# Performance work log

Measured on AMD Instinct MI355X. Metric: run time of the kernel, lower is better.

Reference implementation:

```python
import jax, jax.numpy as jnp
import numpy as np

B, T, C = 4, 2048, 1024
H = 16
D = C // H  # head_dim = 64


def setup_inputs() -> dict:
    key = jax.random.key(0)
    k1, k2, k3 = jax.random.split(key, 3)
    x = jax.random.normal(k1, (B, T, C), dtype=jnp.float32)
    w_qkv = jax.random.normal(k2, (C, 3 * C), dtype=jnp.float32) * (1.0 / np.sqrt(C))
    b_qkv = jnp.zeros((3 * C,), dtype=jnp.float32)
    w_out = jax.random.normal(k3, (C, C), dtype=jnp.float32) * (1.0 / np.sqrt(C))
    b_out = jnp.zeros((C,), dtype=jnp.float32)
    return {"x": x, "w_qkv": w_qkv, "b_qkv": b_qkv, "w_out": w_out, "b_out": b_out}


def reference(x, w_qkv, b_qkv, w_out, b_out):
    # QKV projection: [B,T,3C]
    qkv = x @ w_qkv + b_qkv
    q, k, v = jnp.split(qkv, 3, axis=-1)
    # [B,H,T,D]
    q = q.reshape(B, T, H, D).transpose(0, 2, 1, 3)
    k = k.reshape(B, T, H, D).transpose(0, 2, 1, 3)
    v = v.reshape(B, T, H, D).transpose(0, 2, 1, 3)
    scale = 1.0 / np.sqrt(D)
    # scores: [B,H,T,T]
    scores = jnp.einsum("bhqd,bhkd->bhqk", q, k) * scale
    causal = jnp.tril(jnp.ones((T, T), dtype=bool))
    scores = jnp.where(causal[None, None, :, :], scores, -jnp.inf)
    attn = jax.nn.softmax(scores, axis=-1)
    out = jnp.einsum("bhqk,bhkd->bhqd", attn, v)
    out = out.transpose(0, 2, 1, 3).reshape(B, T, C)
    return out @ w_out + b_out
```

## Files before the change

kernel.cpp:

```cpp
#include <hip/hip_runtime.h>
#include <hip/hip_bf16.h>

#define BB 4
#define TT 2048
#define CC 1024
#define HH 16
#define DD 64

typedef __attribute__((ext_vector_type(8))) short short8;
typedef __attribute__((ext_vector_type(4))) float f32x4;

__device__ __forceinline__ float bf2f(short s) {
  unsigned u = ((unsigned)(unsigned short)s) << 16;
  float f;
  __builtin_memcpy(&f, &u, 4);
  return f;
}
__device__ __forceinline__ short f2bf(float f) {
  unsigned u;
  __builtin_memcpy(&u, &f, 4);
  u = (u + 0x7fffu + ((u >> 16) & 1u)) >> 16;
  return (short)u;
}

__device__ __forceinline__ unsigned cvt_pk_bf16(float lo, float hi) {
  unsigned r;
  asm("v_cvt_pk_bf16_f32 %0, %1, %2" : "=v"(r) : "v"(lo), "v"(hi));
  return r;
}

__device__ __forceinline__ float exp2_fast(float x) {
  float r;
  asm("v_exp_f32 %0, %1" : "=v"(r) : "v"(x));
  return r;
}

template <int CTRL>
__device__ __forceinline__ float dpp_f(float v) {
  union { float f; int i; } u;
  u.f = v;
  u.i = __builtin_amdgcn_update_dpp(0, u.i, CTRL, 0xf, 0xf, true);
  return u.f;
}
__device__ __forceinline__ float rowmax16(float v) {
  v = fmaxf(v, dpp_f<0x128>(v));
  v = fmaxf(v, dpp_f<0x124>(v));
  v = fmaxf(v, dpp_f<0x4E>(v));
  v = fmaxf(v, dpp_f<0xB1>(v));
  return v;
}
__device__ __forceinline__ float rowsum16(float v) {
  v += dpp_f<0x128>(v);
  v += dpp_f<0x124>(v);
  v += dpp_f<0x4E>(v);
  v += dpp_f<0xB1>(v);
  return v;
}

__device__ __forceinline__ void gload_lds16(const void* g, void* l) {
  __builtin_amdgcn_global_load_lds(
      (const __attribute__((address_space(1))) void*)g,
      (__attribute__((address_space(3))) void*)l, 16, 0, 0);
}

__global__ __launch_bounds__(256) void cast_bf16_kernel(
    const float* __restrict__ in, short* __restrict__ out, int n) {
  int i = (blockIdx.x * 256 + threadIdx.x) * 4;
  if (i >= n) return;
  float4 v = *(const float4*)&in[i];
  short4 o;
  o.x = f2bf(v.x); o.y = f2bf(v.y); o.z = f2bf(v.z); o.w = f2bf(v.w);
  *(short4*)&out[i] = o;
}

__global__ __launch_bounds__(256) void transpose_cast_kernel(
    const float* __restrict__ in, short* __restrict__ out, int R, int Cc) {
  __shared__ float tile[32][33];
  const int tx = threadIdx.x, ty = threadIdx.y;
  const int c0 = blockIdx.x * 32, r0 = blockIdx.y * 32;
#pragma unroll
  for (int i = 0; i < 32; i += 8)
    tile[ty + i][tx] = in[(size_t)(r0 + ty + i) * Cc + c0 + tx];
  __syncthreads();
#pragma unroll
  for (int i = 0; i < 32; i += 8)
    out[(size_t)(c0 + ty + i) * R + r0 + tx] = f2bf(tile[tx][ty + i]);
}

__global__ __launch_bounds__(256) void v_transpose_kernel(
    const short* __restrict__ vb, short* __restrict__ vt) {
  __shared__ int tile[32][33];
  const int tx = threadIdx.x, ty = threadIdx.y;
  const int bh = blockIdx.z;
  const int d0 = blockIdx.x * 32, t0 = blockIdx.y * 32;
  const short* src = vb + (size_t)bh * TT * DD;
  short* dstp = vt + (size_t)bh * DD * TT;
#pragma unroll
  for (int i = 0; i < 32; i += 8)
    tile[ty + i][tx] = src[(size_t)(t0 + ty + i) * DD + d0 + tx];
  __syncthreads();
#pragma unroll
  for (int i = 0; i < 32; i += 8)
    dstp[(size_t)(d0 + ty + i) * TT + t0 + tx] = (short)tile[tx][ty + i];
}

template <int MODE>
__global__ __launch_bounds__(256) void gemm_bf16(
    const short* __restrict__ A, const short* __restrict__ Bt,
    const float* __restrict__ bias, float* __restrict__ outF,
    short* __restrict__ outQ, short* __restrict__ outK, short* __restrict__ outV,
    int M, int N, int K) {
  __shared__ __align__(16) short As[2][128 * 32];
  __shared__ __align__(16) short Bs[2][128 * 32];
  const int tid = threadIdx.x;
  const int lane = tid & 63, wid = tid >> 6;
  const int wm = wid >> 1, wn = wid & 1;
  const int nbx = N >> 7;
  const int nwg = nbx * (M >> 7);
  const int lin0 = blockIdx.x;
  const int lin = (lin0 & 7) * (nwg >> 3) + (lin0 >> 3);
  const int bx = lin % nbx, by = lin / nbx;
  const int row0 = by * 128, col0 = bx * 128;
  const int fr = lane & 15, fq = lane >> 4;
  const short* Ab = A + (size_t)row0 * K;
  const short* Bb = Bt + (size_t)col0 * K;
  const int sr = tid >> 2;
  const int so = (tid & 3) * 8;

  f32x4 acc[4][4];
#pragma unroll
  for (int m = 0; m < 4; ++m)
#pragma unroll
    for (int n = 0; n < 4; ++n) {
      f32x4 z = {0.f, 0.f, 0.f, 0.f};
      acc[m][n] = z;
    }

#define GSTAGE(c, k0)                                                          \
  do {                                                                         \
    gload_lds16(Ab + (size_t)sr * K + (k0) + so, &As[c][tid * 8]);             \
    gload_lds16(Ab + (size_t)(sr + 64) * K + (k0) + so, &As[c][2048 + tid * 8]); \
    gload_lds16(Bb + (size_t)sr * K + (k0) + so, &Bs[c][tid * 8]);             \
    gload_lds16(Bb + (size_t)(sr + 64) * K + (k0) + so, &Bs[c][2048 + tid * 8]); \
  } while (0)

  GSTAGE(0, 0);
  const int nkt = K >> 5;
  for (int kt = 0; kt < nkt; ++kt) {
    const int cur = kt & 1;
    asm volatile("s_waitcnt vmcnt(0)" ::: "memory");
    __builtin_amdgcn_s_barrier();
    if (kt + 1 < nkt) GSTAGE(cur ^ 1, (kt + 1) * 32);
    short8 a[4], b[4];
#pragma unroll
    for (int m = 0; m < 4; ++m)
      a[m] = *(const short8*)&As[cur][(wm * 64 + m * 16 + fr) * 32 + fq * 8];
#pragma unroll
    for (int n = 0; n < 4; ++n)
      b[n] = *(const short8*)&Bs[cur][(wn * 64 + n * 16 + fr) * 32 + fq * 8];
    __builtin_amdgcn_s_setprio(1);
#pragma unroll
    for (int m = 0; m < 4; ++m)
#pragma unroll
      for (int n = 0; n < 4; ++n)
        acc[m][n] = __builtin_amdgcn_mfma_f32_16x16x32_bf16(a[m], b[n], acc[m][n], 0, 0, 0);
    __builtin_amdgcn_s_setprio(0);
  }

  float bv[4];
#pragma unroll
  for (int n = 0; n < 4; ++n) bv[n] = bias[col0 + wn * 64 + n * 16 + fr];

  if (MODE == 0) {
#pragma unroll
    for (int m = 0; m < 4; ++m) {
      const int grow = row0 + wm * 64 + m * 16 + fq * 4;
#pragma unroll
      for (int n = 0; n < 4; ++n) {
        const int gcol = col0 + wn * 64 + n * 16 + fr;
#pragma unroll
        for (int r = 0; r < 4; ++r)
          outF[(size_t)(grow + r) * N + gcol] = acc[m][n][r] + bv[n];
      }
    }
  } else {
#pragma unroll
    for (int n = 0; n < 4; ++n) {
      const int gcol = col0 + wn * 64 + n * 16 + fr;
      const int which = gcol >> 10;
      const int h = (gcol & 1023) >> 6;
      const int d = gcol & 63;
      short* dst = (which == 0) ? outQ : (which == 1) ? outK : outV;
#pragma unroll
      for (int m = 0; m < 4; ++m) {
        const int grow = row0 + wm * 64 + m * 16 + fq * 4;
#pragma unroll
        for (int r = 0; r < 4; ++r) {
          const int gb = (grow + r) >> 11;
          const int gt = (grow + r) & 2047;
          const int bh = gb * HH + h;
          dst[((size_t)bh * TT + gt) * DD + d] = f2bf(acc[m][n][r] + bv[n]);
        }
      }
    }
  }
}

#define C2 0.18033688f

__global__ __launch_bounds__(256) void attn_mfma_kernel(
    const short* __restrict__ q,
    const short* __restrict__ k,
    const short* __restrict__ vt,
    short* __restrict__ ctx) {
  __shared__ __align__(16) short Ks[2][128 * 64];
  __shared__ __align__(16) short Vs[2][64 * 128];
  __shared__ __align__(16) short Ps[4][32 * 64];
  const int tid = threadIdx.x, lane = tid & 63, wid = tid >> 6;
  const int fr = lane & 15, fq = lane >> 4;
  const int lin = blockIdx.x;
  const int bh = lin & 63;
  const int qt = 15 - (lin >> 6);
  const int q0 = qt * 128;
  const int qw0 = q0 + wid * 32;
  const short* kbp = k + (size_t)bh * TT * DD;
  const short* vbp = vt + (size_t)bh * DD * TT;
  char* PsB = (char*)&Ps[wid][0];

#define KSB(c) ((char*)&Ks[0][0] + (c) * (128 * 64 * 2))
#define VSB(c) ((char*)&Vs[0][0] + (c) * (64 * 128 * 2))

  short8 aq[2][2];
#pragma unroll
  for (int m = 0; m < 2; ++m)
#pragma unroll
    for (int ks = 0; ks < 2; ++ks)
      aq[m][ks] = *(const short8*)&q[((size_t)bh * TT + qw0 + m * 16 + fr) * DD + ks * 32 + fq * 8];

  float M[2][4], L[2][4];
  f32x4 o[2][4];
#pragma unroll
  for (int m = 0; m < 2; ++m)
#pragma unroll
    for (int r = 0; r < 4; ++r) { M[m][r] = -1e30f; L[m][r] = 0.f; }
#pragma unroll
  for (int m = 0; m < 2; ++m)
#pragma unroll
    for (int dg = 0; dg < 4; ++dg) {
      f32x4 z = {0.f, 0.f, 0.f, 0.f};
      o[m][dg] = z;
    }

  const int nt = qt + 1;

#define STAGE(c, tt)                                                           \
  do {                                                                         \
    const int kv0_ = (tt) * 128;                                               \
    _Pragma("unroll") for (int b_ = 0; b_ < 4; ++b_) {                         \
      const int lo_ = b_ * 4096 + tid * 16;                                    \
      const int row_ = lo_ >> 7;                                               \
      const int colb_ = lo_ & 127;                                             \
      const int src_ = colb_ ^ ((row_ & 7) << 4);                              \
      gload_lds16(kbp + ((size_t)(kv0_ + row_)) * DD + (src_ >> 1),            \
                  KSB(c) + lo_);                                               \
    }                                                                          \
    _Pragma("unroll") for (int b_ = 0; b_ < 4; ++b_) {                         \
      const int lo_ = b_ * 4096 + tid * 16;                                    \
      const int row_ = lo_ >> 8;                                               \
      const int colb_ = lo_ & 255;                                             \
      const int src_ = colb_ ^ ((row_ & 7) << 4);                              \
      gload_lds16(vbp + (size_t)row_ * TT + kv0_ + (src_ >> 1),                \
                  VSB(c) + lo_);                                               \
    }                                                                          \
  } while (0)

  STAGE(0, 0);

  for (int t = 0; t < nt; ++t) {
    const int cur = t & 1;
    asm volatile("s_waitcnt vmcnt(0)" ::: "memory");
    __builtin_amdgcn_s_barrier();
    if (t + 1 < nt) STAGE(cur ^ 1, t + 1);
    const int kv0 = t * 128;
    if (kv0 > qw0 + 31) continue;

#pragma unroll
    for (int sub = 0; sub < 2; ++sub) {
      const int kv0s = kv0 + sub * 64;
      if (kv0s > qw0 + 31) continue;
      const bool domask = (kv0s + 63 > qw0);

      short8 bk[4][2];
#pragma unroll
      for (int n = 0; n < 4; ++n) {
        const int row = sub * 64 + n * 16 + fr;
#pragma unroll
        for (int ks = 0; ks < 2; ++ks)
          bk[n][ks] = *(const short8*)(KSB(cur) + row * 128 +
                                       (((ks * 64 + fq * 16) ^ ((row & 7) << 4))));
      }
      f32x4 s[2][4];
      __builtin_amdgcn_s_setprio(1);
#pragma unroll
      for (int m = 0; m < 2; ++m)
#pragma unroll
        for (int n = 0; n < 4; ++n) {
          f32x4 z = {0.f, 0.f, 0.f, 0.f};
          s[m][n] = z;
#pragma unroll
          for (int ks = 0; ks < 2; ++ks)
            s[m][n] = __builtin_amdgcn_mfma_f32_16x16x32_bf16(aq[m][ks], bk[n][ks], s[m][n], 0, 0, 0);
        }
      __builtin_amdgcn_s_setprio(0);

      if (domask) {
#pragma unroll
        for (int m = 0; m < 2; ++m)
#pragma unroll
          for (int n = 0; n < 4; ++n)
#pragma unroll
            for (int r = 0; r < 4; ++r) {
              const int qq = qw0 + m * 16 + fq * 4 + r;
              const int kk = kv0s + n * 16 + fr;
              if (kk > qq) s[m][n][r] = -1e30f;
            }
      }

#pragma unroll
      for (int m = 0; m < 2; ++m) {
        float rm2[4];
#pragma unroll
        for (int r = 0; r < 4; ++r) {
          float rm = fmaxf(fmaxf(s[m][0][r], s[m][1][r]), fmaxf(s[m][2][r], s[m][3][r]));
          rm2[r] = rowmax16(rm) * C2;
        }
        float dmax = fmaxf(fmaxf(rm2[0] - M[m][0], rm2[1] - M[m][1]),
                           fmaxf(rm2[2] - M[m][2], rm2[3] - M[m][3]));
        if (__any(dmax > 8.0f)) {
#pragma unroll
          for (int r = 0; r < 4; ++r) {
            const float Mn = fmaxf(M[m][r], rm2[r]);
            const float corr = exp2_fast(M[m][r] - Mn);
            M[m][r] = Mn;
            L[m][r] *= corr;
#pragma unroll
            for (int dg = 0; dg < 4; ++dg) o[m][dg][r] *= corr;
          }
        }
        float psum[4] = {0.f, 0.f, 0.f, 0.f};
        const int brow = m * 16 + fq * 4;
        unsigned short* pw = (unsigned short*)PsB;
#pragma unroll
        for (int n = 0; n < 4; ++n) {
          const float p0 = exp2_fast(__builtin_fmaf(s[m][n][0], C2, -M[m][0]));
          const float p1 = exp2_fast(__builtin_fmaf(s[m][n][1], C2, -M[m][1]));
          const float p2 = exp2_fast(__builtin_fmaf(s[m][n][2], C2, -M[m][2]));
          const float p3 = exp2_fast(__builtin_fmaf(s[m][n][3], C2, -M[m][3]));
          psum[0] += p0; psum[1] += p1; psum[2] += p2; psum[3] += p3;
          const unsigned u0 = cvt_pk_bf16(p0, p1);
          const unsigned u1 = cvt_pk_bf16(p2, p3);
          const int colb = n * 32 + fr * 2;
          pw[((brow + 0) * 128 + (colb ^ (((brow + 0) & 7) << 4))) >> 1] = (unsigned short)u0;
          pw[((brow + 1) * 128 + (colb ^ (((brow + 1) & 7) << 4))) >> 1] = (unsigned short)(u0 >> 16);
          pw[((brow + 2) * 128 + (colb ^ (((brow + 2) & 7) << 4))) >> 1] = (unsigned short)u1;
          pw[((brow + 3) * 128 + (colb ^ (((brow + 3) & 7) << 4))) >> 1] = (unsigned short)(u1 >> 16);
        }
#pragma unroll
        for (int r = 0; r < 4; ++r) L[m][r] += rowsum16(psum[r]);
      }

      short8 ap[2][2], bv[4][2];
#pragma unroll
      for (int m = 0; m < 2; ++m) {
        const int qrow = m * 16 + fr;
#pragma unroll
        for (int ks = 0; ks < 2; ++ks)
          ap[m][ks] = *(const short8*)(PsB + qrow * 128 +
                                       (((ks * 64 + fq * 16) ^ ((qrow & 7) << 4))));
      }
#pragma unroll
      for (int dg = 0; dg < 4; ++dg) {
        const int row = dg * 16 + fr;
#pragma unroll
        for (int ks = 0; ks < 2; ++ks)
          bv[dg][ks] = *(const short8*)(VSB(cur) + row * 256 +
                                        (((sub * 128 + ks * 64 + fq * 16) ^ ((row & 7) << 4))));
      }
      __builtin_amdgcn_s_setprio(1);
#pragma unroll
      for (int m = 0; m < 2; ++m)
#pragma unroll
        for (int dg = 0; dg < 4; ++dg)
#pragma unroll
          for (int ks = 0; ks < 2; ++ks)
            o[m][dg] = __builtin_amdgcn_mfma_f32_16x16x32_bf16(ap[m][ks], bv[dg][ks], o[m][dg], 0, 0, 0);
      __builtin_amdgcn_s_setprio(0);
    }
  }

  const int b = bh >> 4, h = bh & 15;
#pragma unroll
  for (int m = 0; m < 2; ++m)
#pragma unroll
    for (int dg = 0; dg < 4; ++dg)
#pragma unroll
      for (int r = 0; r < 4; ++r) {
        const int qq = qw0 + m * 16 + fq * 4 + r;
        ctx[((size_t)(b * TT + qq)) * CC + h * DD + dg * 16 + fr] =
            f2bf(o[m][dg][r] / L[m][r]);
      }
}

extern "C" void kernel_launch(void* const* d_in, const int* in_sizes, int n_in,
                              void* d_out, int out_size, void* d_ws, size_t ws_size,
                              hipStream_t stream) {
  (void)in_sizes; (void)n_in; (void)out_size; (void)ws_size;
  const float* x = (const float*)d_in[0];
  const float* w_qkv = (const float*)d_in[1];
  const float* b_qkv = (const float*)d_in[2];
  const float* w_out = (const float*)d_in[3];
  const float* b_out = (const float*)d_in[4];
  float* out = (float*)d_out;

  char* w = (char*)d_ws;
  short* xb    = (short*)w; w += (size_t)BB * TT * CC * 2;
  short* wqkvT = (short*)w; w += (size_t)3 * CC * CC * 2;
  short* woutT = (short*)w; w += (size_t)CC * CC * 2;
  short* qb    = (short*)w; w += (size_t)BB * HH * TT * DD * 2;
  short* kb    = (short*)w; w += (size_t)BB * HH * TT * DD * 2;
  short* vtb   = (short*)w; w += (size_t)BB * HH * DD * TT * 2;
  short* ctx   = (short*)w; w += (size_t)BB * TT * CC * 2;

  const int M = BB * TT;

  cast_bf16_kernel<<<dim3((M * CC) / 4 / 256), dim3(256), 0, stream>>>(x, xb, M * CC);
  transpose_cast_kernel<<<dim3(3 * CC / 32, CC / 32), dim3(32, 8), 0, stream>>>(
      w_qkv, wqkvT, CC, 3 * CC);
  transpose_cast_kernel<<<dim3(CC / 32, CC / 32), dim3(32, 8), 0, stream>>>(
      w_out, woutT, CC, CC);

  gemm_bf16<1><<<dim3((3 * CC / 128) * (M / 128)), dim3(256), 0, stream>>>(
      xb, wqkvT, b_qkv, nullptr, qb, kb, ctx, M, 3 * CC, CC);

  v_transpose_kernel<<<dim3(DD / 32, TT / 32, BB * HH), dim3(32, 8), 0, stream>>>(
      ctx, vtb);

  attn_mfma_kernel<<<dim3(16 * 64), dim3(256), 0, stream>>>(qb, kb, vtb, ctx);

  gemm_bf16<0><<<dim3((CC / 128) * (M / 128)), dim3(256), 0, stream>>>(
      ctx, woutT, b_out, out, nullptr, nullptr, nullptr, M, CC, CC);
}
```

Measured before the change: 287.8 us.

## Swizzle GEMM LDS tiles and shrink attention KV tiles to 64

```diff
diff --git a/kernel.cpp b/kernel.cpp
--- a/kernel.cpp
+++ b/kernel.cpp
@@ -125,7 +125,8 @@
   const short* Ab = A + (size_t)row0 * K;
   const short* Bb = Bt + (size_t)col0 * K;
   const int sr = tid >> 2;
-  const int so = (tid & 3) * 8;
+  const int ssl = (((tid & 3) ^ (sr & 3)) * 8);
+  const int rsl = ((fq ^ (fr & 3)) * 8);
 
   f32x4 acc[4][4];
 #pragma unroll
@@ -136,12 +137,12 @@
       acc[m][n] = z;
     }
 
-#define GSTAGE(c, k0)                                                          \
-  do {                                                                         \
-    gload_lds16(Ab + (size_t)sr * K + (k0) + so, &As[c][tid * 8]);             \
-    gload_lds16(Ab + (size_t)(sr + 64) * K + (k0) + so, &As[c][2048 + tid * 8]); \
-    gload_lds16(Bb + (size_t)sr * K + (k0) + so, &Bs[c][tid * 8]);             \
-    gload_lds16(Bb + (size_t)(sr + 64) * K + (k0) + so, &Bs[c][2048 + tid * 8]); \
+#define GSTAGE(c, k0)                                                            \
+  do {                                                                           \
+    gload_lds16(Ab + (size_t)sr * K + (k0) + ssl, &As[c][tid * 8]);              \
+    gload_lds16(Ab + (size_t)(sr + 64) * K + (k0) + ssl, &As[c][2048 + tid * 8]);\
+    gload_lds16(Bb + (size_t)sr * K + (k0) + ssl, &Bs[c][tid * 8]);              \
+    gload_lds16(Bb + (size_t)(sr + 64) * K + (k0) + ssl, &Bs[c][2048 + tid * 8]);\
   } while (0)
 
   GSTAGE(0, 0);
@@ -154,10 +155,10 @@
     short8 a[4], b[4];
 #pragma unroll
     for (int m = 0; m < 4; ++m)
-      a[m] = *(const short8*)&As[cur][(wm * 64 + m * 16 + fr) * 32 + fq * 8];
+      a[m] = *(const short8*)&As[cur][(wm * 64 + m * 16 + fr) * 32 + rsl];
 #pragma unroll
     for (int n = 0; n < 4; ++n)
-      b[n] = *(const short8*)&Bs[cur][(wn * 64 + n * 16 + fr) * 32 + fq * 8];
+      b[n] = *(const short8*)&Bs[cur][(wn * 64 + n * 16 + fr) * 32 + rsl];
     __builtin_amdgcn_s_setprio(1);
 #pragma unroll
     for (int m = 0; m < 4; ++m)
@@ -213,8 +214,8 @@
     const short* __restrict__ k,
     const short* __restrict__ vt,
     short* __restrict__ ctx) {
-  __shared__ __align__(16) short Ks[2][128 * 64];
-  __shared__ __align__(16) short Vs[2][64 * 128];
+  __shared__ __align__(16) short Ks[2][64 * 64];
+  __shared__ __align__(16) short Vs[2][64 * 64];
   __shared__ __align__(16) short Ps[4][32 * 64];
   const int tid = threadIdx.x, lane = tid & 63, wid = tid >> 6;
   const int fr = lane & 15, fq = lane >> 4;
@@ -227,8 +228,8 @@
   const short* vbp = vt + (size_t)bh * DD * TT;
   char* PsB = (char*)&Ps[wid][0];
 
-#define KSB(c) ((char*)&Ks[0][0] + (c) * (128 * 64 * 2))
-#define VSB(c) ((char*)&Vs[0][0] + (c) * (64 * 128 * 2))
+#define KSB(c) ((char*)&Ks[0][0] + (c) * (64 * 64 * 2))
+#define VSB(c) ((char*)&Vs[0][0] + (c) * (64 * 64 * 2))
 
   short8 aq[2][2];
 #pragma unroll
@@ -251,26 +252,24 @@
       o[m][dg] = z;
     }
 
-  const int nt = qt + 1;
+  const int nt = 2 * qt + 2;
 
 #define STAGE(c, tt)                                                           \
   do {                                                                         \
-    const int kv0_ = (tt) * 128;                                               \
-    _Pragma("unroll") for (int b_ = 0; b_ < 4; ++b_) {                         \
+    const int kv0_ = (tt) * 64;                                                \
+    _Pragma("unroll") for (int b_ = 0; b_ < 2; ++b_) {                         \
       const int lo_ = b_ * 4096 + tid * 16;                                    \
       const int row_ = lo_ >> 7;                                               \
       const int colb_ = lo_ & 127;                                             \
-      const int src_ = colb_ ^ ((row_ & 7) << 4);                              \
-      gload_lds16(kbp + ((size_t)(kv0_ + row_)) * DD + (src_ >> 1),            \
-                  KSB(c) + lo_);                                               \
+      const int src_ = (colb_ ^ ((row_ & 7) << 4)) >> 1;                       \
+      gload_lds16(kbp + ((size_t)(kv0_ + row_)) * DD + src_, KSB(c) + lo_);    \
     }                                                                          \
-    _Pragma("unroll") for (int b_ = 0; b_ < 4; ++b_) {                         \
+    _Pragma("unroll") for (int b_ = 0; b_ < 2; ++b_) {                         \
       const int lo_ = b_ * 4096 + tid * 16;                                    \
-      const int row_ = lo_ >> 8;                                               \
-      const int colb_ = lo_ & 255;                                             \
-      const int src_ = colb_ ^ ((row_ & 7) << 4);                              \
-      gload_lds16(vbp + (size_t)row_ * TT + kv0_ + (src_ >> 1),                \
-                  VSB(c) + lo_);                                               \
+      const int row_ = lo_ >> 7;                                               \
+      const int colb_ = lo_ & 127;                                             \
+      const int src_ = (colb_ ^ ((row_ & 7) << 4)) >> 1;                       \
+      gload_lds16(vbp + (size_t)row_ * TT + kv0_ + src_, VSB(c) + lo_);        \
     }                                                                          \
   } while (0)
 
@@ -281,121 +280,115 @@
     asm volatile("s_waitcnt vmcnt(0)" ::: "memory");
     __builtin_amdgcn_s_barrier();
     if (t + 1 < nt) STAGE(cur ^ 1, t + 1);
-    const int kv0 = t * 128;
-    if (kv0 > qw0 + 31) continue;
-
-#pragma unroll
-    for (int sub = 0; sub < 2; ++sub) {
-      const int kv0s = kv0 + sub * 64;
-      if (kv0s > qw0 + 31) continue;
-      const bool domask = (kv0s + 63 > qw0);
-
-      short8 bk[4][2];
+    const int kv0s = t * 64;
+    if (kv0s > qw0 + 31) continue;
+    const bool domask = (kv0s + 63 > qw0);
+
+    short8 bk[4][2];
+#pragma unroll
+    for (int n = 0; n < 4; ++n) {
+      const int row = n * 16 + fr;
+#pragma unroll
+      for (int ks = 0; ks < 2; ++ks)
+        bk[n][ks] = *(const short8*)(KSB(cur) + row * 128 +
+                                     (((ks * 64 + fq * 16) ^ ((row & 7) << 4))));
+    }
+    f32x4 s[2][4];
+    __builtin_amdgcn_s_setprio(1);
+#pragma unroll
+    for (int m = 0; m < 2; ++m)
 #pragma unroll
       for (int n = 0; n < 4; ++n) {
-        const int row = sub * 64 + n * 16 + fr;
+        f32x4 z = {0.f, 0.f, 0.f, 0.f};
+        s[m][n] = z;
 #pragma unroll
         for (int ks = 0; ks < 2; ++ks)
-          bk[n][ks] = *(const short8*)(KSB(cur) + row * 128 +
+          s[m][n] = __builtin_amdgcn_mfma_f32_16x16x32_bf16(aq[m][ks], bk[n][ks], s[m][n], 0, 0, 0);
+      }
+    __builtin_amdgcn_s_setprio(0);
+
+    if (domask) {
+#pragma unroll
+      for (int m = 0; m < 2; ++m)
+#pragma unroll
+        for (int n = 0; n < 4; ++n)
+#pragma unroll
+          for (int r = 0; r < 4; ++r) {
+            const int qq = qw0 + m * 16 + fq * 4 + r;
+            const int kk = kv0s + n * 16 + fr;
+            if (kk > qq) s[m][n][r] = -1e30f;
+          }
+    }
+
+#pragma unroll
+    for (int m = 0; m < 2; ++m) {
+      float rm2[4];
+#pragma unroll
+      for (int r = 0; r < 4; ++r) {
+        float rm = fmaxf(fmaxf(s[m][0][r], s[m][1][r]), fmaxf(s[m][2][r], s[m][3][r]));
+        rm2[r] = rowmax16(rm) * C2;
+      }
+      float dmax = fmaxf(fmaxf(rm2[0] - M[m][0], rm2[1] - M[m][1]),
+                         fmaxf(rm2[2] - M[m][2], rm2[3] - M[m][3]));
+      if (__any(dmax > 8.0f)) {
+#pragma unroll
+        for (int r = 0; r < 4; ++r) {
+          const float Mn = fmaxf(M[m][r], rm2[r]);
+          const float corr = exp2_fast(M[m][r] - Mn);
+          M[m][r] = Mn;
+          L[m][r] *= corr;
+#pragma unroll
+          for (int dg = 0; dg < 4; ++dg) o[m][dg][r] *= corr;
+        }
+      }
+      float psum[4] = {0.f, 0.f, 0.f, 0.f};
+      const int brow = m * 16 + fq * 4;
+      unsigned short* pw = (unsigned short*)PsB;
+#pragma unroll
+      for (int n = 0; n < 4; ++n) {
+        const float p0 = exp2_fast(__builtin_fmaf(s[m][n][0], C2, -M[m][0]));
+        const float p1 = exp2_fast(__builtin_fmaf(s[m][n][1], C2, -M[m][1]));
+        const float p2 = exp2_fast(__builtin_fmaf(s[m][n][2], C2, -M[m][2]));
+        const float p3 = exp2_fast(__builtin_fmaf(s[m][n][3], C2, -M[m][3]));
+        psum[0] += p0; psum[1] += p1; psum[2] += p2; psum[3] += p3;
+        const unsigned u0 = cvt_pk_bf16(p0, p1);
+        const unsigned u1 = cvt_pk_bf16(p2, p3);
+        const int colb = n * 32 + fr * 2;
+        pw[((brow + 0) * 128 + (colb ^ (((brow + 0) & 7) << 4))) >> 1] = (unsigned short)u0;
+        pw[((brow + 1) * 128 + (colb ^ (((brow + 1) & 7) << 4))) >> 1] = (unsigned short)(u0 >> 16);
+        pw[((brow + 2) * 128 + (colb ^ (((brow + 2) & 7) << 4))) >> 1] = (unsigned short)u1;
+        pw[((brow + 3) * 128 + (colb ^ (((brow + 3) & 7) << 4))) >> 1] = (unsigned short)(u1 >> 16);
+      }
+#pragma unroll
+      for (int r = 0; r < 4; ++r) L[m][r] += rowsum16(psum[r]);
+    }
+
+    short8 ap[2][2], bvv[4][2];
+#pragma unroll
+    for (int m = 0; m < 2; ++m) {
+      const int qrow = m * 16 + fr;
+#pragma unroll
+      for (int ks = 0; ks < 2; ++ks)
+        ap[m][ks] = *(const short8*)(PsB + qrow * 128 +
+                                     (((ks * 64 + fq * 16) ^ ((qrow & 7) << 4))));
+    }
+#pragma unroll
+    for (int dg = 0; dg < 4; ++dg) {
+      const int row = dg * 16 + fr;
+#pragma unroll
+      for (int ks = 0; ks < 2; ++ks)
+        bvv[dg][ks] = *(const short8*)(VSB(cur) + row * 128 +
                                        (((ks * 64 + fq * 16) ^ ((row & 7) << 4))));
-      }
-      f32x4 s[2][4];
-      __builtin_amdgcn_s_setprio(1);
-#pragma unroll
-      for (int m = 0; m < 2; ++m)
-#pragma unroll
-        for (int n = 0; n < 4; ++n) {
-          f32x4 z = {0.f, 0.f, 0.f, 0.f};
-          s[m][n] = z;
-#pragma unroll
-          for (int ks = 0; ks < 2; ++ks)
-            s[m][n] = __builtin_amdgcn_mfma_f32_16x16x32_bf16(aq[m][ks], bk[n][ks], s[m][n], 0, 0, 0);
-        }
-      __builtin_amdgcn_s_setprio(0);
-
-      if (domask) {
-#pragma unroll
-        for (int m = 0; m < 2; ++m)
-#pragma unroll
-          for (int n = 0; n < 4; ++n)
-#pragma unroll
-            for (int r = 0; r < 4; ++r) {
-              const int qq = qw0 + m * 16 + fq * 4 + r;
-              const int kk = kv0s + n * 16 + fr;
-              if (kk > qq) s[m][n][r] = -1e30f;
-            }
-      }
-
-#pragma unroll
-      for (int m = 0; m < 2; ++m) {
-        float rm2[4];
-#pragma unroll
-        for (int r = 0; r < 4; ++r) {
-          float rm = fmaxf(fmaxf(s[m][0][r], s[m][1][r]), fmaxf(s[m][2][r], s[m][3][r]));
-          rm2[r] = rowmax16(rm) * C2;
-        }
-        float dmax = fmaxf(fmaxf(rm2[0] - M[m][0], rm2[1] - M[m][1]),
-                           fmaxf(rm2[2] - M[m][2], rm2[3] - M[m][3]));
-        if (__any(dmax > 8.0f)) {
-#pragma unroll
-          for (int r = 0; r < 4; ++r) {
-            const float Mn = fmaxf(M[m][r], rm2[r]);
-            const float corr = exp2_fast(M[m][r] - Mn);
-            M[m][r] = Mn;
-            L[m][r] *= corr;
-#pragma unroll
-            for (int dg = 0; dg < 4; ++dg) o[m][dg][r] *= corr;
-          }
-        }
-        float psum[4] = {0.f, 0.f, 0.f, 0.f};
-        const int brow = m * 16 + fq * 4;
-        unsigned short* pw = (unsigned short*)PsB;
-#pragma unroll
-        for (int n = 0; n < 4; ++n) {
-          const float p0 = exp2_fast(__builtin_fmaf(s[m][n][0], C2, -M[m][0]));
-          const float p1 = exp2_fast(__builtin_fmaf(s[m][n][1], C2, -M[m][1]));
-          const float p2 = exp2_fast(__builtin_fmaf(s[m][n][2], C2, -M[m][2]));
-          const float p3 = exp2_fast(__builtin_fmaf(s[m][n][3], C2, -M[m][3]));
-          psum[0] += p0; psum[1] += p1; psum[2] += p2; psum[3] += p3;
-          const unsigned u0 = cvt_pk_bf16(p0, p1);
-          const unsigned u1 = cvt_pk_bf16(p2, p3);
-          const int colb = n * 32 + fr * 2;
-          pw[((brow + 0) * 128 + (colb ^ (((brow + 0) & 7) << 4))) >> 1] = (unsigned short)u0;
-          pw[((brow + 1) * 128 + (colb ^ (((brow + 1) & 7) << 4))) >> 1] = (unsigned short)(u0 >> 16);
-          pw[((brow + 2) * 128 + (colb ^ (((brow + 2) & 7) << 4))) >> 1] = (unsigned short)u1;
-          pw[((brow + 3) * 128 + (colb ^ (((brow + 3) & 7) << 4))) >> 1] = (unsigned short)(u1 >> 16);
-        }
-#pragma unroll
-        for (int r = 0; r < 4; ++r) L[m][r] += rowsum16(psum[r]);
-      }
-
-      short8 ap[2][2], bv[4][2];
-#pragma unroll
-      for (int m = 0; m < 2; ++m) {
-        const int qrow = m * 16 + fr;
+    }
+    __builtin_amdgcn_s_setprio(1);
+#pragma unroll
+    for (int m = 0; m < 2; ++m)
+#pragma unroll
+      for (int dg = 0; dg < 4; ++dg)
 #pragma unroll
         for (int ks = 0; ks < 2; ++ks)
-          ap[m][ks] = *(const short8*)(PsB + qrow * 128 +
-                                       (((ks * 64 + fq * 16) ^ ((qrow & 7) << 4))));
-      }
-#pragma unroll
-      for (int dg = 0; dg < 4; ++dg) {
-        const int row = dg * 16 + fr;
-#pragma unroll
-        for (int ks = 0; ks < 2; ++ks)
-          bv[dg][ks] = *(const short8*)(VSB(cur) + row * 256 +
-                                        (((sub * 128 + ks * 64 + fq * 16) ^ ((row & 7) << 4))));
-      }
-      __builtin_amdgcn_s_setprio(1);
-#pragma unroll
-      for (int m = 0; m < 2; ++m)
-#pragma unroll
-        for (int dg = 0; dg < 4; ++dg)
-#pragma unroll
-          for (int ks = 0; ks < 2; ++ks)
-            o[m][dg] = __builtin_amdgcn_mfma_f32_16x16x32_bf16(ap[m][ks], bv[dg][ks], o[m][dg], 0, 0, 0);
-      __builtin_amdgcn_s_setprio(0);
-    }
+          o[m][dg] = __builtin_amdgcn_mfma_f32_16x16x32_bf16(ap[m][ks], bvv[dg][ks], o[m][dg], 0, 0, 0);
+    __builtin_amdgcn_s_setprio(0);
   }
 
   const int b = bh >> 4, h = bh & 15;
```

Measured after the change: 295.5 us. 2.7% more time.
